# Kernel optimization log

Hardware: AMD Instinct MI355X
Metric: run time of the kernel (lower is better)

The kernel has to match this reference:

```python
import jax, jax.numpy as jnp
import numpy as np

B, C, H, W = 16, 192, 64, 64
L = 256           # number of quantization levels (len(sos.unique_values))
EXTREMA = 10.0    # codebook support roughly [-extrema, extrema]


def setup_inputs() -> dict:
    key = jax.random.key(0)
    k1, k2, k3 = jax.random.split(key, 3)
    inputs = jax.random.normal(k1, (B, C, H, W), dtype=jnp.float32) * 3.0
    means = jax.random.normal(k2, (B, C, H, W), dtype=jnp.float32)
    # sorted codebook of unique quantizer output values (sos.unique_values)
    raw = jax.random.uniform(k3, (L,), dtype=jnp.float32,
                             minval=-EXTREMA, maxval=EXTREMA)
    unique_values = jnp.sort(raw)
    return {"inputs": inputs, "means": means, "unique_values": unique_values}


def _nearest_symbols(v, unique_values):
    # Parallel binary search over the sorted codebook; equivalent to the
    # original per-element argmin(|keys - x|) in transform_map.
    L_ = unique_values.shape[0]
    idx = jnp.searchsorted(unique_values, v)          # in [0, L]
    idx = jnp.clip(idx, 1, L_ - 1)
    left = unique_values[idx - 1]
    right = unique_values[idx]
    # on ties, argmin picks the lower index -> use <=
    return jnp.where(jnp.abs(v - left) <= jnp.abs(v - right), idx - 1, idx)


def reference(inputs, means, unique_values):
    # quantize(mode='symbols'): subtract means, snap to nearest codebook
    # value, map value -> integer symbol via the sorted codebook.
    v = inputs - means
    symbols = _nearest_symbols(v, unique_values)      # int32 [B,C,H,W]
    # dequantize: symbol -> float codebook value (map_cdf_sos), add means.
    dequant = unique_values[symbols] + means          # float32 [B,C,H,W]
    return dequant, symbols
```

## Files before the change

kernel.cpp:

```cpp
#include <hip/hip_runtime.h>


#define LVL 256
#define NB  2048
#define MAINBLOCKS 2048

__global__ __launch_bounds__(256) void agc_build_lut(
    const float* __restrict__ uv, float* __restrict__ ws)
{
    __shared__ float s_uv[LVL];
    if (threadIdx.x < LVL) s_uv[threadIdx.x] = uv[threadIdx.x];
    __syncthreads();

    int b = blockIdx.x * blockDim.x + threadIdx.x;
    if (b >= NB) return;

    float lo    = s_uv[0];
    float width = (s_uv[LVL - 1] - lo) / (float)NB;

    float eL = (b == 0)      ? -__builtin_inff() : lo + (float)(b - 1) * width;
    float eU = (b == NB - 1) ?  __builtin_inff() : lo + (float)(b + 2) * width;

    int A, Bc;
    {
        int l = 0, h = LVL;
        #pragma unroll
        for (int s = 0; s < 8; ++s) {
            int m = (l + h) >> 1;
            bool r = (s_uv[m] < eL);
            l = r ? (m + 1) : l;
            h = r ? h : m;
        }
        A = l;
        l = 0; h = LVL;
        #pragma unroll
        for (int s = 0; s < 8; ++s) {
            int m = (l + h) >> 1;
            bool r = (s_uv[m] < eU);
            l = r ? (m + 1) : l;
            h = r ? h : m;
        }
        Bc = l;
    }
    int cA = min(max(A, 1), LVL - 1);
    int cB = min(max(Bc, 1), LVL - 1);

    float* lutL = ws;
    float* lutR = ws + NB;
    int*   lutS = reinterpret_cast<int*>(ws + 2 * NB);

    if (cA == cB) {
        lutL[b] = s_uv[cA - 1];
        lutR[b] = s_uv[cA];
        lutS[b] = cA - 1;
    } else {
        lutL[b] = 0.0f;
        lutR[b] = 0.0f;
        lutS[b] = -(A + 1);
    }
}

__global__ __launch_bounds__(256) void agc_quant_lut(
    const float* __restrict__ inputs,
    const float* __restrict__ means,
    const float* __restrict__ uv,
    const float* __restrict__ ws,
    float* __restrict__ out_deq,
    float* __restrict__ out_sym,
    int n4, int n, int stride)
{
    __shared__ float s_uv[LVL];
    __shared__ float s_L[NB];
    __shared__ float s_R[NB];
    __shared__ int   s_S[NB];

    s_uv[threadIdx.x] = uv[threadIdx.x];
    {
        const float4* wL = reinterpret_cast<const float4*>(ws);
        const float4* wR = reinterpret_cast<const float4*>(ws + NB);
        const int4*   wS = reinterpret_cast<const int4*>(ws + 2 * NB);
        #pragma unroll
        for (int t = 0; t < NB / 4 / 256; ++t) {
            int j = t * 256 + threadIdx.x;
            reinterpret_cast<float4*>(s_L)[j] = wL[j];
            reinterpret_cast<float4*>(s_R)[j] = wR[j];
            reinterpret_cast<int4*>(s_S)[j]   = wS[j];
        }
    }
    __syncthreads();

    const float lo    = s_uv[0];
    const float scale = (float)NB / (s_uv[LVL - 1] - lo);

    for (int i = blockIdx.x * blockDim.x + threadIdx.x; i < n4; i += stride) {
        float4 in = reinterpret_cast<const float4*>(inputs)[i];
        float4 mn = reinterpret_cast<const float4*>(means)[i];

        float vs[4] = {in.x - mn.x, in.y - mn.y, in.z - mn.z, in.w - mn.w};
        float ms[4] = {mn.x, mn.y, mn.z, mn.w};
        float dq[4], sy[4];

        #pragma unroll
        for (int k = 0; k < 4; ++k) {
            float v = vs[k];
            int b = (int)floorf((v - lo) * scale);
            b = min(max(b, 0), NB - 1);

            float left  = s_L[b];
            float right = s_R[b];
            int   code  = s_S[b];
            int   base  = code;

            if (code < 0) {
                int s = -code - 1;
                while (s < LVL && s_uv[s] < v) ++s;
                int idx = min(max(s, 1), LVL - 1);
                left  = s_uv[idx - 1];
                right = s_uv[idx];
                base  = idx - 1;
            }

            bool tl = (fabsf(v - left) <= fabsf(v - right));
            sy[k] = (float)(tl ? base : base + 1);
            dq[k] = (tl ? left : right) + ms[k];
        }

        reinterpret_cast<float4*>(out_deq)[i] = make_float4(dq[0], dq[1], dq[2], dq[3]);
        reinterpret_cast<float4*>(out_sym)[i] = make_float4(sy[0], sy[1], sy[2], sy[3]);
    }

    if (blockIdx.x == 0 && threadIdx.x == 0) {
        for (int j = n4 * 4; j < n; ++j) {
            float m = means[j];
            float v = inputs[j] - m;
            int l = 0, h = LVL;
            for (int s = 0; s < 8; ++s) {
                int mm = (l + h) >> 1;
                bool r = (s_uv[mm] < v);
                l = r ? (mm + 1) : l;
                h = r ? h : mm;
            }
            int idx = min(max(l, 1), LVL - 1);
            float left = s_uv[idx - 1], right = s_uv[idx];
            bool tl = fabsf(v - left) <= fabsf(v - right);
            out_deq[j] = (tl ? left : right) + m;
            out_sym[j] = (float)(tl ? idx - 1 : idx);
        }
    }
}

__global__ __launch_bounds__(256) void agc_quant_fallback(
    const float* __restrict__ inputs,
    const float* __restrict__ means,
    const float* __restrict__ uv,
    float* __restrict__ out_deq,
    float* __restrict__ out_sym,
    int n4, int n)
{
    __shared__ float s_uv[LVL];
    s_uv[threadIdx.x] = uv[threadIdx.x];
    __syncthreads();

    int i = blockIdx.x * blockDim.x + threadIdx.x;
    if (i < n4) {
        float4 in = reinterpret_cast<const float4*>(inputs)[i];
        float4 mn = reinterpret_cast<const float4*>(means)[i];
        float vs[4] = {in.x - mn.x, in.y - mn.y, in.z - mn.z, in.w - mn.w};
        float ms[4] = {mn.x, mn.y, mn.z, mn.w};
        float dq[4], sy[4];
        #pragma unroll
        for (int k = 0; k < 4; ++k) {
            float v = vs[k];
            int lo = 0, hi = LVL;
            #pragma unroll
            for (int s = 0; s < 8; ++s) {
                int mid = (lo + hi) >> 1;
                bool r = (s_uv[mid] < v);
                lo = r ? (mid + 1) : lo;
                hi = r ? hi : mid;
            }
            int idx = min(max(lo, 1), LVL - 1);
            float left = s_uv[idx - 1], right = s_uv[idx];
            bool tl = (fabsf(v - left) <= fabsf(v - right));
            sy[k] = (float)(tl ? idx - 1 : idx);
            dq[k] = (tl ? left : right) + ms[k];
        }
        reinterpret_cast<float4*>(out_deq)[i] = make_float4(dq[0], dq[1], dq[2], dq[3]);
        reinterpret_cast<float4*>(out_sym)[i] = make_float4(sy[0], sy[1], sy[2], sy[3]);
    }
    if (blockIdx.x == 0 && threadIdx.x == 0) {
        for (int j = n4 * 4; j < n; ++j) {
            float m = means[j];
            float v = inputs[j] - m;
            int lo = 0, hi = LVL;
            for (int s = 0; s < 8; ++s) {
                int mid = (lo + hi) >> 1;
                bool r = (s_uv[mid] < v);
                lo = r ? (mid + 1) : lo;
                hi = r ? hi : mid;
            }
            int idx = min(max(lo, 1), LVL - 1);
            float left = s_uv[idx - 1], right = s_uv[idx];
            bool tl = fabsf(v - left) <= fabsf(v - right);
            out_deq[j] = (tl ? left : right) + m;
            out_sym[j] = (float)(tl ? idx - 1 : idx);
        }
    }
}

extern "C" void kernel_launch(void* const* d_in, const int* in_sizes, int n_in,
                              void* d_out, int out_size, void* d_ws, size_t ws_size,
                              hipStream_t stream)
{
    const float* inputs = (const float*)d_in[0];
    const float* means  = (const float*)d_in[1];
    const float* uv     = (const float*)d_in[2];

    int n  = in_sizes[0];
    int n4 = n / 4;

    float* out     = (float*)d_out;
    float* out_deq = out;
    float* out_sym = out + n;

    size_t need = (size_t)NB * 3 * sizeof(float);
    if (d_ws != nullptr && ws_size >= need) {
        agc_build_lut<<<NB / 256, 256, 0, stream>>>(uv, (float*)d_ws);

        int blocks = (n4 + 255) / 256;
        if (blocks > MAINBLOCKS) blocks = MAINBLOCKS;
        if (blocks < 1)          blocks = 1;
        agc_quant_lut<<<blocks, 256, 0, stream>>>(
            inputs, means, uv, (const float*)d_ws,
            out_deq, out_sym, n4, n, blocks * 256);
    } else {
        int blocks = (n4 + 255) / 256;
        if (blocks < 1) blocks = 1;
        agc_quant_fallback<<<blocks, 256, 0, stream>>>(
            inputs, means, uv, out_deq, out_sym, n4, n);
    }
}
```

Baseline: 184.9 us.

## Pack LUT into float4 entries, halve bucket count, batch loads per thread

Rebuilds the bucket lookup table as one float4 per bucket (left, right, base index, packed fallback range) with 1024 buckets, built by a single block that counts how many codebook values fall in each bucket. The main kernel stages this smaller table into shared memory with one vector read per lookup and issues four independent input/means loads per thread before computing, instead of a grid-stride loop. The intent is to cut the per-block LUT staging cost and the shared-memory reads per element, and to raise memory-level parallelism. The cost is more buckets that fall back to a linear scan of the codebook.

```diff
diff --git a/kernel.cpp b/kernel.cpp
--- a/kernel.cpp
+++ b/kernel.cpp
@@ -2,61 +2,49 @@
 
 
 #define LVL 256
-#define NB  2048
-#define MAINBLOCKS 2048
+#define NB  1024
+#define QPT 4
+
+__device__ __forceinline__ int bucket_of(float v, float lo, float scale) {
+    int b = (int)floorf((v - lo) * scale);
+    return min(max(b, 0), NB - 1);
+}
 
 __global__ __launch_bounds__(256) void agc_build_lut(
-    const float* __restrict__ uv, float* __restrict__ ws)
+    const float* __restrict__ uv, float4* __restrict__ lut)
 {
     __shared__ float s_uv[LVL];
-    if (threadIdx.x < LVL) s_uv[threadIdx.x] = uv[threadIdx.x];
-    __syncthreads();
-
-    int b = blockIdx.x * blockDim.x + threadIdx.x;
-    if (b >= NB) return;
-
-    float lo    = s_uv[0];
-    float width = (s_uv[LVL - 1] - lo) / (float)NB;
-
-    float eL = (b == 0)      ? -__builtin_inff() : lo + (float)(b - 1) * width;
-    float eU = (b == NB - 1) ?  __builtin_inff() : lo + (float)(b + 2) * width;
-
-    int A, Bc;
-    {
-        int l = 0, h = LVL;
-        #pragma unroll
-        for (int s = 0; s < 8; ++s) {
-            int m = (l + h) >> 1;
-            bool r = (s_uv[m] < eL);
-            l = r ? (m + 1) : l;
-            h = r ? h : m;
-        }
-        A = l;
-        l = 0; h = LVL;
-        #pragma unroll
-        for (int s = 0; s < 8; ++s) {
-            int m = (l + h) >> 1;
-            bool r = (s_uv[m] < eU);
-            l = r ? (m + 1) : l;
-            h = r ? h : m;
-        }
-        Bc = l;
-    }
-    int cA = min(max(A, 1), LVL - 1);
-    int cB = min(max(Bc, 1), LVL - 1);
-
-    float* lutL = ws;
-    float* lutR = ws + NB;
-    int*   lutS = reinterpret_cast<int*>(ws + 2 * NB);
-
-    if (cA == cB) {
-        lutL[b] = s_uv[cA - 1];
-        lutR[b] = s_uv[cA];
-        lutS[b] = cA - 1;
-    } else {
-        lutL[b] = 0.0f;
-        lutR[b] = 0.0f;
-        lutS[b] = -(A + 1);
+    __shared__ int   s_b[LVL];
+    int t = threadIdx.x;
+    s_uv[t] = uv[t];
+    __syncthreads();
+    const float lo    = s_uv[0];
+    const float scale = (float)NB / (s_uv[LVL - 1] - lo);
+    s_b[t] = bucket_of(s_uv[t], lo, scale);
+    __syncthreads();
+
+    #pragma unroll
+    for (int q = 0; q < NB / 256; ++q) {
+        int b = q * 256 + t;
+        int A = 0, cnt = 0;
+        for (int j = 0; j < LVL; ++j) {
+            int bj = s_b[j];
+            A   += (bj <  b);
+            cnt += (bj == b);
+        }
+        float4 e;
+        if (cnt == 0) {
+            int idx = min(max(A, 1), LVL - 1);
+            e.x = s_uv[idx - 1];
+            e.y = s_uv[idx];
+            e.z = (float)(idx - 1);
+            e.w = 0.0f;
+        } else {
+            unsigned w = 0x80000000u | ((unsigned)A << 10) | (unsigned)cnt;
+            e.x = 0.0f; e.y = 0.0f; e.z = 0.0f;
+            e.w = __int_as_float((int)w);
+        }
+        lut[b] = e;
     }
 }
 
@@ -64,72 +52,78 @@
     const float* __restrict__ inputs,
     const float* __restrict__ means,
     const float* __restrict__ uv,
-    const float* __restrict__ ws,
+    const float4* __restrict__ lut,
     float* __restrict__ out_deq,
     float* __restrict__ out_sym,
-    int n4, int n, int stride)
-{
-    __shared__ float s_uv[LVL];
-    __shared__ float s_L[NB];
-    __shared__ float s_R[NB];
-    __shared__ int   s_S[NB];
-
-    s_uv[threadIdx.x] = uv[threadIdx.x];
-    {
-        const float4* wL = reinterpret_cast<const float4*>(ws);
-        const float4* wR = reinterpret_cast<const float4*>(ws + NB);
-        const int4*   wS = reinterpret_cast<const int4*>(ws + 2 * NB);
-        #pragma unroll
-        for (int t = 0; t < NB / 4 / 256; ++t) {
-            int j = t * 256 + threadIdx.x;
-            reinterpret_cast<float4*>(s_L)[j] = wL[j];
-            reinterpret_cast<float4*>(s_R)[j] = wR[j];
-            reinterpret_cast<int4*>(s_S)[j]   = wS[j];
-        }
-    }
+    int n4, int n, int gstride)
+{
+    __shared__ float  s_uv[LVL];
+    __shared__ float4 s_lut[NB];
+
+    int t = threadIdx.x;
+    s_uv[t] = uv[t];
+    #pragma unroll
+    for (int q = 0; q < NB / 256; ++q)
+        s_lut[q * 256 + t] = lut[q * 256 + t];
     __syncthreads();
 
     const float lo    = s_uv[0];
     const float scale = (float)NB / (s_uv[LVL - 1] - lo);
 
-    for (int i = blockIdx.x * blockDim.x + threadIdx.x; i < n4; i += stride) {
-        float4 in = reinterpret_cast<const float4*>(inputs)[i];
-        float4 mn = reinterpret_cast<const float4*>(means)[i];
-
-        float vs[4] = {in.x - mn.x, in.y - mn.y, in.z - mn.z, in.w - mn.w};
-        float ms[4] = {mn.x, mn.y, mn.z, mn.w};
+    const int base = blockIdx.x * blockDim.x + t;
+
+    float4 in[QPT], mn[QPT];
+    bool   ok[QPT];
+    #pragma unroll
+    for (int k = 0; k < QPT; ++k) {
+        int i = base + k * gstride;
+        ok[k] = (i < n4);
+        if (ok[k]) {
+            in[k] = reinterpret_cast<const float4*>(inputs)[i];
+            mn[k] = reinterpret_cast<const float4*>(means)[i];
+        }
+    }
+
+    #pragma unroll
+    for (int k = 0; k < QPT; ++k) {
+        if (!ok[k]) continue;
+        int i = base + k * gstride;
+
+        float vs[4] = {in[k].x - mn[k].x, in[k].y - mn[k].y,
+                       in[k].z - mn[k].z, in[k].w - mn[k].w};
+        float ms[4] = {mn[k].x, mn[k].y, mn[k].z, mn[k].w};
         float dq[4], sy[4];
 
         #pragma unroll
-        for (int k = 0; k < 4; ++k) {
-            float v = vs[k];
-            int b = (int)floorf((v - lo) * scale);
-            b = min(max(b, 0), NB - 1);
-
-            float left  = s_L[b];
-            float right = s_R[b];
-            int   code  = s_S[b];
-            int   base  = code;
-
-            if (code < 0) {
-                int s = -code - 1;
-                while (s < LVL && s_uv[s] < v) ++s;
+        for (int e4 = 0; e4 < 4; ++e4) {
+            float v = vs[e4];
+            int b = bucket_of(v, lo, scale);
+
+            float4 e = s_lut[b];
+            int w = __float_as_int(e.w);
+            float left = e.x, right = e.y, basef = e.z;
+
+            if (w < 0) {
+                int A   = (w >> 10) & 0x3FF;
+                int cnt =  w        & 0x3FF;
+                int s = A, end = A + cnt;
+                while (s < end && s_uv[s] < v) ++s;
                 int idx = min(max(s, 1), LVL - 1);
                 left  = s_uv[idx - 1];
                 right = s_uv[idx];
-                base  = idx - 1;
+                basef = (float)(idx - 1);
             }
 
             bool tl = (fabsf(v - left) <= fabsf(v - right));
-            sy[k] = (float)(tl ? base : base + 1);
-            dq[k] = (tl ? left : right) + ms[k];
+            sy[e4] = tl ? basef : basef + 1.0f;
+            dq[e4] = (tl ? left : right) + ms[e4];
         }
 
         reinterpret_cast<float4*>(out_deq)[i] = make_float4(dq[0], dq[1], dq[2], dq[3]);
         reinterpret_cast<float4*>(out_sym)[i] = make_float4(sy[0], sy[1], sy[2], sy[3]);
     }
 
-    if (blockIdx.x == 0 && threadIdx.x == 0) {
+    if (blockIdx.x == 0 && t == 0) {
         for (int j = n4 * 4; j < n; ++j) {
             float m = means[j];
             float v = inputs[j] - m;
@@ -223,16 +217,17 @@
     float* out_deq = out;
     float* out_sym = out + n;
 
-    size_t need = (size_t)NB * 3 * sizeof(float);
+    size_t need = (size_t)NB * sizeof(float4);
     if (d_ws != nullptr && ws_size >= need) {
-        agc_build_lut<<<NB / 256, 256, 0, stream>>>(uv, (float*)d_ws);
-
-        int blocks = (n4 + 255) / 256;
-        if (blocks > MAINBLOCKS) blocks = MAINBLOCKS;
-        if (blocks < 1)          blocks = 1;
+        agc_build_lut<<<1, 256, 0, stream>>>(uv, (float4*)d_ws);
+
+        long long per_blk = 256LL * QPT;
+        int blocks = (int)((n4 + per_blk - 1) / per_blk);
+        if (blocks < 1) blocks = 1;
+        int gstride = blocks * 256;
         agc_quant_lut<<<blocks, 256, 0, stream>>>(
-            inputs, means, uv, (const float*)d_ws,
-            out_deq, out_sym, n4, n, blocks * 256);
+            inputs, means, uv, (const float4*)d_ws,
+            out_deq, out_sym, n4, n, gstride);
     } else {
         int blocks = (n4 + 255) / 256;
         if (blocks < 1) blocks = 1;
```

Measured after the change: 201.2 us. 8.8% more time.
